# Kernel optimization log

Measured on AMD Instinct MI355X. Metric: run time of the kernel, lower is better.

The kernel has to match this reference:

```python
import jax, jax.numpy as jnp
import numpy as np

B, N0, N1, N2, HS, NCLS = 16384, 57, 20, 10, 5, 17
EPS = 1e-4  # SPDRectified eigenvalue floor
_TRI = np.triu_indices(HS)  # upper-tri vectorization indices


def _bilinear(x, W):
    # SPDTransform: W^T X W, W: (in, out) column-orthonormal (Stiefel)
    return jnp.einsum('ji,bjk,kl->bil', W, x, W)


def _rectify(x):
    # SPDRectified: eigh, clamp eigenvalues at EPS, recompose
    w, v = jnp.linalg.eigh(x)
    w = jnp.maximum(w, EPS)
    return jnp.einsum('bij,bj,bkj->bik', v, w, v)


def _logmap(x):
    # SPDTangentSpace log map: eigh, log eigenvalues, recompose
    w, v = jnp.linalg.eigh(x)
    w = jnp.log(w)
    return jnp.einsum('bij,bj,bkj->bik', v, w, v)


def setup_inputs() -> dict:
    key = jax.random.key(0)
    ks = jax.random.split(key, 6)
    A = jax.random.normal(ks[0], (B, N0, N0), dtype=jnp.float32)
    # SPD input: A A^T / N0 + 0.01 I
    x = jnp.einsum('bij,bkj->bik', A, A) / N0 + 0.01 * jnp.eye(N0, dtype=jnp.float32)

    def stiefel(k, m, n):
        q, _ = jnp.linalg.qr(jax.random.normal(k, (m, n), dtype=jnp.float32))
        return q  # (m, n) column-orthonormal

    W1 = stiefel(ks[1], N0, N1)
    W2 = stiefel(ks[2], N1, N2)
    W3 = stiefel(ks[3], N2, HS)
    tri = HS * (HS + 1) // 2
    lin_w = jax.random.normal(ks[4], (NCLS, tri), dtype=jnp.float32) / np.sqrt(tri)
    lin_b = jax.random.normal(ks[5], (NCLS,), dtype=jnp.float32) * 0.01
    return {"x": x, "W1": W1, "W2": W2, "W3": W3, "lin_w": lin_w, "lin_b": lin_b}


def reference(x, W1, W2, W3, lin_w, lin_b):
    x = _rectify(_bilinear(x, W1))   # [B,20,20]
    x = _rectify(_bilinear(x, W2))   # [B,10,10]
    x = _rectify(_bilinear(x, W3))   # [B,HS,HS]
    x = _logmap(x)                   # tangent space
    vec = x[:, _TRI[0], _TRI[1]]     # [B, HS*(HS+1)/2]
    return vec @ lin_w.T + lin_b     # [B, 17]
```

## Files before the change

kernel.cpp:

```cpp
#include <hip/hip_runtime.h>
#include <math.h>

#define BATCH 16384
#define N0 57
#define NX 3249
#define GPB 4
#define HS 5
#define NCLS 17
#define NTRI 15
#define EPSV 1e-4f

template<int CTRL>
__device__ __forceinline__ float dpp_mov0(float x) {
    return __int_as_float(__builtin_amdgcn_update_dpp(
        0, __float_as_int(x), CTRL, 0xF, 0xF, true));
}
__device__ __forceinline__ float wave_sum64(float x) {
    x += dpp_mov0<0x111>(x);
    x += dpp_mov0<0x112>(x);
    x += dpp_mov0<0x114>(x);
    x += dpp_mov0<0x118>(x);
    x += dpp_mov0<0x142>(x);
    x += dpp_mov0<0x143>(x);
    return x;
}

__device__ __forceinline__ void load_lds16(const float* g, float* l) {
    __builtin_amdgcn_global_load_lds(
        (const __attribute__((address_space(1))) void*)g,
        (__attribute__((address_space(3))) void*)l, 16, 0, 0);
}

__global__ __launch_bounds__(256) void k_main(const float* __restrict__ x,
                                              const float* __restrict__ W1,
                                              const float* __restrict__ W2,
                                              const float* __restrict__ W3,
                                              float* __restrict__ y_out) {
    __shared__ float xs[13312];
    __shared__ float wcsT[304];
    __shared__ float w23[100];
    const int tid  = threadIdx.x;
    const int lane = tid & 63;
    const int wave = tid >> 6;

    float w2r[10], w3c[10], w1r[20];
    const int kk = tid / 5, jj = tid % 5;
    if (tid < 100) {
        #pragma unroll
        for (int l = 0; l < 10; ++l) { w2r[l] = W2[kk * 10 + l]; w3c[l] = W3[l * HS + jj]; }
    }
    if (tid < N0) {
        const float4* w1p = (const float4*)(W1 + tid * 20);
        #pragma unroll
        for (int q = 0; q < 5; ++q) {
            float4 v = w1p[q];
            w1r[4*q] = v.x; w1r[4*q+1] = v.y; w1r[4*q+2] = v.z; w1r[4*q+3] = v.w;
        }
    }
    if (tid < 304) wcsT[tid] = 0.f;

    const float* gbase = x + (size_t)blockIdx.x * (GPB * NX);
    #pragma unroll
    for (int r = 0; r < 13; ++r) {
        int slot = r * 256 + tid;
        int cs = slot > 3248 ? 3248 : slot;
        load_lds16(gbase + (size_t)cs * 4, &xs[r * 1024 + (tid & 192) * 4]);
    }

    if (tid < 100) {
        float acc = 0.f;
        #pragma unroll
        for (int l = 0; l < 10; ++l) acc = fmaf(w2r[l], w3c[l], acc);
        w23[tid] = acc;
    }
    asm volatile("s_waitcnt lgkmcnt(0)" ::: "memory");
    __builtin_amdgcn_s_barrier();

    if (tid < N0) {
        #pragma unroll
        for (int j = 0; j < HS; ++j) {
            float acc = 0.f;
            #pragma unroll
            for (int k = 0; k < 20; ++k) acc = fmaf(w1r[k], w23[k * HS + j], acc);
            wcsT[j * 60 + tid] = acc;
        }
    }

    asm volatile("s_waitcnt vmcnt(0) lgkmcnt(0)" ::: "memory");
    __builtin_amdgcn_s_barrier();

    const int la = (lane < N0) ? lane : 56;
    const float* row = &xs[wave * NX + la * N0];
    float wv[HS];
    #pragma unroll
    for (int j = 0; j < HS; ++j) {
        float v = wcsT[j * 60 + lane];
        wv[j] = (lane < N0) ? v : 0.f;
    }
    float s[HS] = {0.f, 0.f, 0.f, 0.f, 0.f};
    #pragma unroll
    for (int c = 0; c < 14; ++c) {
        float r0 = row[4*c], r1 = row[4*c+1], r2 = row[4*c+2], r3 = row[4*c+3];
        #pragma unroll
        for (int j = 0; j < HS; ++j) {
            float4 w4 = *(const float4*)&wcsT[j * 60 + 4 * c];
            s[j] = fmaf(r0, w4.x, fmaf(r1, w4.y, fmaf(r2, w4.z, fmaf(r3, w4.w, s[j]))));
        }
    }
    {
        float r56 = row[56];
        #pragma unroll
        for (int j = 0; j < HS; ++j) s[j] = fmaf(r56, wcsT[j * 60 + 56], s[j]);
    }

    float p[NTRI];
    int t = 0;
    #pragma unroll
    for (int i = 0; i < HS; ++i)
        #pragma unroll
        for (int j = i; j < HS; ++j) { p[t] = wave_sum64(wv[i] * s[j]); ++t; }

    if (lane == 63) {
        float4* o = (float4*)&y_out[(size_t)(blockIdx.x * GPB + wave) * 16];
        o[0] = make_float4(p[0],  p[1],  p[2],  p[3]);
        o[1] = make_float4(p[4],  p[5],  p[6],  p[7]);
        o[2] = make_float4(p[8],  p[9],  p[10], p[11]);
        o[3] = make_float4(p[12], p[13], p[14], 0.f);
    }
}

__global__ __launch_bounds__(256) void k_eig(const float* __restrict__ y_in,
                                             const float* __restrict__ lin_w,
                                             const float* __restrict__ lin_b,
                                             float* __restrict__ out) {
    __shared__ float lws[NCLS * NTRI];
    __shared__ float lbs[NCLS];
    int tid = threadIdx.x;
    if (tid < NCLS * NTRI) lws[tid] = lin_w[tid];
    if (tid < NCLS) lbs[tid] = lin_b[tid];
    __syncthreads();

    int m = blockIdx.x * 256 + tid;
    const float4* yin = (const float4*)&y_in[(size_t)m * 16];
    float4 q0 = yin[0], q1 = yin[1], q2 = yin[2], q3 = yin[3];
    float tri[16] = {q0.x, q0.y, q0.z, q0.w, q1.x, q1.y, q1.z, q1.w,
                     q2.x, q2.y, q2.z, q2.w, q3.x, q3.y, q3.z, q3.w};

    float A[HS][HS], V[HS][HS];
    int t = 0;
    #pragma unroll
    for (int i = 0; i < HS; ++i)
        #pragma unroll
        for (int j = i; j < HS; ++j) { A[i][j] = tri[t]; A[j][i] = tri[t]; ++t; }
    #pragma unroll
    for (int i = 0; i < HS; ++i)
        #pragma unroll
        for (int j = 0; j < HS; ++j) V[i][j] = (i == j) ? 1.f : 0.f;

    #pragma unroll
    for (int sweep = 0; sweep < 6; ++sweep) {
        #pragma unroll
        for (int p = 0; p < HS - 1; ++p) {
            #pragma unroll
            for (int q = p + 1; q < HS; ++q) {
                float apq = A[p][q];
                float app = A[p][p], aqq = A[q][q];
                bool nz = fabsf(apq) > 1e-30f;
                float denom = nz ? 2.f * apq : 1.f;
                float tau = (aqq - app) / denom;
                float tt = 1.f / (fabsf(tau) + sqrtf(fmaf(tau, tau, 1.f)));
                tt = copysignf(tt, tau);
                tt = nz ? tt : 0.f;
                float c = rsqrtf(fmaf(tt, tt, 1.f));
                float sn = tt * c;
                #pragma unroll
                for (int k = 0; k < HS; ++k) {
                    float akp = A[k][p], akq = A[k][q];
                    A[k][p] = fmaf(c, akp, -sn * akq);
                    A[k][q] = fmaf(sn, akp,  c * akq);
                }
                #pragma unroll
                for (int k = 0; k < HS; ++k) {
                    float apk = A[p][k], aqk = A[q][k];
                    A[p][k] = fmaf(c, apk, -sn * aqk);
                    A[q][k] = fmaf(sn, apk,  c * aqk);
                }
                #pragma unroll
                for (int k = 0; k < HS; ++k) {
                    float vkp = V[k][p], vkq = V[k][q];
                    V[k][p] = fmaf(c, vkp, -sn * vkq);
                    V[k][q] = fmaf(sn, vkp,  c * vkq);
                }
            }
        }
    }

    float lwv[HS];
    #pragma unroll
    for (int i = 0; i < HS; ++i) lwv[i] = logf(fmaxf(A[i][i], EPSV));

    float tri2[NTRI];
    t = 0;
    #pragma unroll
    for (int i = 0; i < HS; ++i) {
        float vi[HS];
        #pragma unroll
        for (int k = 0; k < HS; ++k) vi[k] = V[i][k] * lwv[k];
        #pragma unroll
        for (int j = i; j < HS; ++j) {
            float acc = 0.f;
            #pragma unroll
            for (int k = 0; k < HS; ++k) acc = fmaf(vi[k], V[j][k], acc);
            tri2[t++] = acc;
        }
    }

    #pragma unroll
    for (int c = 0; c < NCLS; ++c) {
        float acc = lbs[c];
        #pragma unroll
        for (int k = 0; k < NTRI; ++k) acc = fmaf(tri2[k], lws[c * NTRI + k], acc);
        out[(size_t)m * NCLS + c] = acc;
    }
}

extern "C" void kernel_launch(void* const* d_in, const int* in_sizes, int n_in,
                              void* d_out, int out_size, void* d_ws, size_t ws_size,
                              hipStream_t stream) {
    const float* x     = (const float*)d_in[0];
    const float* W1    = (const float*)d_in[1];
    const float* W2    = (const float*)d_in[2];
    const float* W3    = (const float*)d_in[3];
    const float* lin_w = (const float*)d_in[4];
    const float* lin_b = (const float*)d_in[5];
    float* out = (float*)d_out;
    float* y   = (float*)d_ws;

    k_main<<<BATCH / GPB, 256, 0, stream>>>(x, W1, W2, W3, y);
    k_eig<<<BATCH / 256, 256, 0, stream>>>(y, lin_w, lin_b, out);
}
```

Baseline: 58.52 us.

## Hoist combined weight product into setup kernel and shrink eig block size

Moves the W1·W2·W3 product into a separate one-block setup kernel that writes it to workspace, so each main block no longer recomputes it or needs an extra barrier. The main kernel now reads x column-wise with lane-contiguous LDS access and takes the weights from global memory through uniform loads. The eigen kernel uses 64-thread blocks so more blocks exist to spread over CUs. In exchange it adds a third kernel launch, and the per-element global weight reads in the inner loop rely on scalar caching.

```diff
diff --git a/kernel.cpp b/kernel.cpp
--- a/kernel.cpp
+++ b/kernel.cpp
@@ -31,33 +31,50 @@
         (__attribute__((address_space(3))) void*)l, 16, 0, 0);
 }
 
+__global__ __launch_bounds__(128) void k_setup(const float* __restrict__ W1,
+                                               const float* __restrict__ W2,
+                                               const float* __restrict__ W3,
+                                               float* __restrict__ wc_out) {
+    __shared__ float w23[100];
+    int t = threadIdx.x;
+    if (t < 100) {
+        int k = t / 5, j = t % 5;
+        float acc = 0.f;
+        for (int l = 0; l < 10; ++l) acc = fmaf(W2[k * 10 + l], W3[l * 5 + j], acc);
+        w23[t] = acc;
+    }
+    __syncthreads();
+    if (t < N0) {
+        float r[5];
+        #pragma unroll
+        for (int j = 0; j < 5; ++j) {
+            float acc = 0.f;
+            for (int k = 0; k < 20; ++k) acc = fmaf(W1[t * 20 + k], w23[k * 5 + j], acc);
+            r[j] = acc;
+        }
+        float4* o = (float4*)&wc_out[t * 8];
+        o[0] = make_float4(r[0], r[1], r[2], r[3]);
+        o[1] = make_float4(r[4], 0.f, 0.f, 0.f);
+    }
+}
+
 __global__ __launch_bounds__(256) void k_main(const float* __restrict__ x,
-                                              const float* __restrict__ W1,
-                                              const float* __restrict__ W2,
-                                              const float* __restrict__ W3,
+                                              const float* __restrict__ wc,
                                               float* __restrict__ y_out) {
     __shared__ float xs[13312];
-    __shared__ float wcsT[304];
-    __shared__ float w23[100];
     const int tid  = threadIdx.x;
     const int lane = tid & 63;
     const int wave = tid >> 6;
 
-    float w2r[10], w3c[10], w1r[20];
-    const int kk = tid / 5, jj = tid % 5;
-    if (tid < 100) {
-        #pragma unroll
-        for (int l = 0; l < 10; ++l) { w2r[l] = W2[kk * 10 + l]; w3c[l] = W3[l * HS + jj]; }
-    }
-    if (tid < N0) {
-        const float4* w1p = (const float4*)(W1 + tid * 20);
-        #pragma unroll
-        for (int q = 0; q < 5; ++q) {
-            float4 v = w1p[q];
-            w1r[4*q] = v.x; w1r[4*q+1] = v.y; w1r[4*q+2] = v.z; w1r[4*q+3] = v.w;
-        }
-    }
-    if (tid < 304) wcsT[tid] = 0.f;
+    float wv[HS];
+    {
+        int a = (lane < N0) ? lane : 0;
+        const float4* wp = (const float4*)&wc[a * 8];
+        float4 v0 = wp[0];
+        float  v4 = wc[a * 8 + 4];
+        wv[0] = v0.x; wv[1] = v0.y; wv[2] = v0.z; wv[3] = v0.w; wv[4] = v4;
+        if (lane >= N0) { wv[0] = wv[1] = wv[2] = wv[3] = wv[4] = 0.f; }
+    }
 
     const float* gbase = x + (size_t)blockIdx.x * (GPB * NX);
     #pragma unroll
@@ -67,50 +84,16 @@
         load_lds16(gbase + (size_t)cs * 4, &xs[r * 1024 + (tid & 192) * 4]);
     }
 
-    if (tid < 100) {
-        float acc = 0.f;
-        #pragma unroll
-        for (int l = 0; l < 10; ++l) acc = fmaf(w2r[l], w3c[l], acc);
-        w23[tid] = acc;
-    }
-    asm volatile("s_waitcnt lgkmcnt(0)" ::: "memory");
+    asm volatile("s_waitcnt vmcnt(0)" ::: "memory");
     __builtin_amdgcn_s_barrier();
 
-    if (tid < N0) {
-        #pragma unroll
-        for (int j = 0; j < HS; ++j) {
-            float acc = 0.f;
-            #pragma unroll
-            for (int k = 0; k < 20; ++k) acc = fmaf(w1r[k], w23[k * HS + j], acc);
-            wcsT[j * 60 + tid] = acc;
-        }
-    }
-
-    asm volatile("s_waitcnt vmcnt(0) lgkmcnt(0)" ::: "memory");
-    __builtin_amdgcn_s_barrier();
-
-    const int la = (lane < N0) ? lane : 56;
-    const float* row = &xs[wave * NX + la * N0];
-    float wv[HS];
-    #pragma unroll
-    for (int j = 0; j < HS; ++j) {
-        float v = wcsT[j * 60 + lane];
-        wv[j] = (lane < N0) ? v : 0.f;
-    }
+    const float* base = &xs[wave * NX];
     float s[HS] = {0.f, 0.f, 0.f, 0.f, 0.f};
     #pragma unroll
-    for (int c = 0; c < 14; ++c) {
-        float r0 = row[4*c], r1 = row[4*c+1], r2 = row[4*c+2], r3 = row[4*c+3];
-        #pragma unroll
-        for (int j = 0; j < HS; ++j) {
-            float4 w4 = *(const float4*)&wcsT[j * 60 + 4 * c];
-            s[j] = fmaf(r0, w4.x, fmaf(r1, w4.y, fmaf(r2, w4.z, fmaf(r3, w4.w, s[j]))));
-        }
-    }
-    {
-        float r56 = row[56];
-        #pragma unroll
-        for (int j = 0; j < HS; ++j) s[j] = fmaf(r56, wcsT[j * 60 + 56], s[j]);
+    for (int b = 0; b < N0; ++b) {
+        float xv = base[b * N0 + lane];
+        #pragma unroll
+        for (int j = 0; j < HS; ++j) s[j] = fmaf(xv, wc[b * 8 + j], s[j]);
     }
 
     float p[NTRI];
@@ -129,18 +112,18 @@
     }
 }
 
-__global__ __launch_bounds__(256) void k_eig(const float* __restrict__ y_in,
-                                             const float* __restrict__ lin_w,
-                                             const float* __restrict__ lin_b,
-                                             float* __restrict__ out) {
+__global__ __launch_bounds__(64) void k_eig(const float* __restrict__ y_in,
+                                            const float* __restrict__ lin_w,
+                                            const float* __restrict__ lin_b,
+                                            float* __restrict__ out) {
     __shared__ float lws[NCLS * NTRI];
     __shared__ float lbs[NCLS];
     int tid = threadIdx.x;
-    if (tid < NCLS * NTRI) lws[tid] = lin_w[tid];
+    for (int i = tid; i < NCLS * NTRI; i += 64) lws[i] = lin_w[i];
     if (tid < NCLS) lbs[tid] = lin_b[tid];
     __syncthreads();
 
-    int m = blockIdx.x * 256 + tid;
+    int m = blockIdx.x * 64 + tid;
     const float4* yin = (const float4*)&y_in[(size_t)m * 16];
     float4 q0 = yin[0], q1 = yin[1], q2 = yin[2], q3 = yin[3];
     float tri[16] = {q0.x, q0.y, q0.z, q0.w, q1.x, q1.y, q1.z, q1.w,
@@ -234,8 +217,11 @@
     const float* lin_w = (const float*)d_in[4];
     const float* lin_b = (const float*)d_in[5];
     float* out = (float*)d_out;
-    float* y   = (float*)d_ws;
-
-    k_main<<<BATCH / GPB, 256, 0, stream>>>(x, W1, W2, W3, y);
-    k_eig<<<BATCH / 256, 256, 0, stream>>>(y, lin_w, lin_b, out);
-}
+    float* ws  = (float*)d_ws;
+    float* wc  = ws;
+    float* y   = ws + 512;
+
+    k_setup<<<1, 128, 0, stream>>>(W1, W2, W3, wc);
+    k_main<<<BATCH / GPB, 256, 0, stream>>>(x, wc, y);
+    k_eig<<<BATCH / 64, 64, 0, stream>>>(y, lin_w, lin_b, out);
+}
```

Result: no change. 58.35 us (-0.3%).
